# Optimization experiments

Measured on AMD Instinct MI355X. Metric: run time of the kernel, lower is better.

The kernel has to match this reference:

```python
import jax, jax.numpy as jnp
import numpy as np

N_NODES = 100000


def gcn_conv(x, W, b, src, dst, n):
    # PyG GCNConv: linear transform, add self-loops, symmetric degree norm, scatter-add, bias
    h = x @ W                                      # [n, d_out]
    loop = jnp.arange(n, dtype=src.dtype)
    s = jnp.concatenate([src, loop])               # [E + n]
    d = jnp.concatenate([dst, loop])
    deg = jax.ops.segment_sum(jnp.ones_like(d, dtype=h.dtype), d, num_segments=n)
    dinv = jnp.where(deg > 0, jax.lax.rsqrt(deg), 0.0)
    norm = dinv[s] * dinv[d]                       # [E + n]
    msg = h[s] * norm[:, None]                     # gather + scale
    out = jax.ops.segment_sum(msg, d, num_segments=n)  # scatter-add over targets
    return out + b


def setup_inputs() -> dict:
    key = jax.random.key(0)
    ks = jax.random.split(key, 8)
    n, c_in, hid, c_out = N_NODES, 256, 128, 64
    x = jax.random.normal(ks[0], (n, c_in), dtype=jnp.float32)
    edge_index = jax.random.randint(ks[1], (2, 1600000), 0, n, dtype=jnp.int64)
    s = 0.1
    return {
        "x": x,
        "edge_index": edge_index,
        "W1": jax.random.normal(ks[2], (c_in, hid), dtype=jnp.float32) * s,
        "b1": jnp.zeros((hid,), dtype=jnp.float32),
        "Wmu": jax.random.normal(ks[3], (hid, c_out), dtype=jnp.float32) * s,
        "bmu": jnp.zeros((c_out,), dtype=jnp.float32),
        "Wlv": jax.random.normal(ks[4], (hid, c_out), dtype=jnp.float32) * s,
        "blv": jnp.zeros((c_out,), dtype=jnp.float32),
    }


def reference(x, edge_index, W1, b1, Wmu, bmu, Wlv, blv):
    n = x.shape[0]
    src, dst = edge_index[0], edge_index[1]
    h = jax.nn.relu(gcn_conv(x, W1, b1, src, dst, n))
    mu = gcn_conv(h, Wmu, bmu, src, dst, n)
    logvar = gcn_conv(h, Wlv, blv, src, dst, n)
    return mu, logvar
```

## Files before the change

### kernel.cpp

```cpp
#include <hip/hip_runtime.h>


#define C_IN  256
#define HID   128
#define C_OUT 64
#define NBUCK 1024
#define P1WGS 256

typedef __attribute__((ext_vector_type(8))) short bf16x8;
typedef __attribute__((ext_vector_type(4))) float f32x4;

__device__ inline unsigned short f2bf(float f) {
  unsigned u = __float_as_uint(f);
  unsigned r = u + 0x7FFF + ((u >> 16) & 1);
  return (unsigned short)(r >> 16);
}
__device__ inline float bflo(unsigned v) { return __uint_as_float(v << 16); }
__device__ inline float bfhi(unsigned v) { return __uint_as_float(v & 0xFFFF0000u); }

__global__ __launch_bounds__(256) void k_bin_count(const int* __restrict__ dst,
                                                   int* __restrict__ histmat, int E) {
  __shared__ int h[NBUCK];
  int tid = threadIdx.x;
  for (int i = tid; i < NBUCK; i += 256) h[i] = 0;
  __syncthreads();
  for (int e = blockIdx.x * 256 + tid; e < E; e += P1WGS * 256)
    atomicAdd(&h[dst[e] >> 7], 1);
  __syncthreads();
  for (int i = tid; i < NBUCK; i += 256)
    histmat[blockIdx.x * NBUCK + i] = h[i];
}

__global__ __launch_bounds__(256) void k_col_scan(int* __restrict__ histmat,
                                                  int* __restrict__ bucket_tot) {
  __shared__ int sh[P1WGS];
  int b = blockIdx.x;
  int t = threadIdx.x;
  int v = histmat[t * NBUCK + b];
  sh[t] = v; __syncthreads();
  for (int ofs = 1; ofs < P1WGS; ofs <<= 1) {
    int add = (t >= ofs) ? sh[t - ofs] : 0;
    __syncthreads();
    sh[t] += add;
    __syncthreads();
  }
  histmat[t * NBUCK + b] = sh[t] - v;
  if (t == P1WGS - 1) bucket_tot[b] = sh[t];
}

__global__ void k_bucket_scan(const int* __restrict__ bucket_tot,
                              int* __restrict__ bucket_start, int E) {
  __shared__ int sh[NBUCK];
  int t = threadIdx.x;
  int v = bucket_tot[t];
  sh[t] = v; __syncthreads();
  for (int ofs = 1; ofs < NBUCK; ofs <<= 1) {
    int add = (t >= ofs) ? sh[t - ofs] : 0;
    __syncthreads();
    sh[t] += add;
    __syncthreads();
  }
  bucket_start[t] = sh[t] - v;
  if (t == NBUCK - 1) bucket_start[NBUCK] = E;
}

__global__ __launch_bounds__(256) void k_bin_scatter(const int* __restrict__ src,
                                                     const int* __restrict__ dst,
                                                     const int* __restrict__ histmat,
                                                     const int* __restrict__ bucket_start,
                                                     unsigned* __restrict__ binned, int E) {
  __shared__ int cur[NBUCK];
  int tid = threadIdx.x;
  for (int i = tid; i < NBUCK; i += 256)
    cur[i] = bucket_start[i] + histmat[blockIdx.x * NBUCK + i];
  __syncthreads();
  for (int e = blockIdx.x * 256 + tid; e < E; e += P1WGS * 256) {
    int d = dst[e];
    int pos = atomicAdd(&cur[d >> 7], 1);
    binned[pos] = (unsigned)src[e] | ((unsigned)(d & 127) << 17);
  }
}

__global__ __launch_bounds__(256) void k_bucket_csr(const unsigned* __restrict__ binned,
                                                    const int* __restrict__ bucket_start,
                                                    int* __restrict__ row_start,
                                                    float* __restrict__ dinv,
                                                    int* __restrict__ csr_src,
                                                    int n, int E) {
  __shared__ int h[128], ls[128], c[128];
  int b = blockIdx.x, t = threadIdx.x;
  int start = bucket_start[b], end = bucket_start[b + 1];
  if (t < 128) h[t] = 0;
  __syncthreads();
  for (int e = start + t; e < end; e += 256)
    atomicAdd(&h[binned[e] >> 17], 1);
  __syncthreads();
  if (t < 128) ls[t] = h[t];
  __syncthreads();
  for (int ofs = 1; ofs < 128; ofs <<= 1) {
    int add = (t < 128 && t >= ofs) ? ls[t - ofs] : 0;
    __syncthreads();
    if (t < 128) ls[t] += add;
    __syncthreads();
  }
  if (t < 128) {
    int excl = ls[t] - h[t];
    ls[t] = excl;
    c[t] = excl;
    int node = b * 128 + t;
    if (node < n) {
      row_start[node] = start + excl;
      dinv[node] = rsqrtf((float)h[t] + 1.0f);
    }
  }
  if (b == 0 && t == 0) row_start[n] = E;
  __syncthreads();
  for (int e = start + t; e < end; e += 256) {
    unsigned v = binned[e];
    int pos = start + atomicAdd(&c[v >> 17], 1);
    csr_src[pos] = (int)(v & 0x1FFFF);
  }
}

__global__ void k_prep(const float* __restrict__ W1, const float* __restrict__ Wmu,
                       const float* __restrict__ Wlv,
                       unsigned short* __restrict__ bswz1,
                       unsigned short* __restrict__ bswz2,
                       unsigned* __restrict__ p1z, unsigned* __restrict__ p2z) {
  int idx = blockIdx.x * 256 + threadIdx.x;
  if (idx < 4096) {
    int L = idx & 63, t = (idx >> 6) & 7, s = idx >> 9;
    const float* srcp = W1 + (size_t)(s * 32 + ((L >> 4) << 3)) * 128 + t * 16 + (L & 15);
    unsigned short* dstp = bswz1 + (size_t)idx * 8;
#pragma unroll
    for (int j = 0; j < 8; j++) dstp[j] = f2bf(srcp[(size_t)j * 128]);
  } else if (idx < 6144) {
    int id2 = idx - 4096;
    int L = id2 & 63, t = (id2 >> 6) & 7, s = id2 >> 9;
    int nn = t * 16 + (L & 15);
    int k0 = s * 32 + ((L >> 4) << 3);
    const float* W = (nn < C_OUT) ? (Wmu + nn) : (Wlv + (nn - C_OUT));
    unsigned short* dstp = bswz2 + (size_t)id2 * 8;
#pragma unroll
    for (int j = 0; j < 8; j++) dstp[j] = f2bf(W[(size_t)(k0 + j) * C_OUT]);
  } else if (idx < 6208) {
    p1z[idx - 6144] = 0u;
  } else if (idx < 6272) {
    p2z[idx - 6208] = 0u;
  }
}

template <typename AT, int K>
__global__ __launch_bounds__(256) void k_gemm_mfma(const AT* __restrict__ A,
                                                   const unsigned short* __restrict__ bswz,
                                                   unsigned short* __restrict__ C,
                                                   const float* __restrict__ dinv,
                                                   int M) {
  constexpr int NS = K / 32;
  int wave = threadIdx.x >> 6, lane = threadIdx.x & 63;
  int m0 = blockIdx.x * 64 + wave * 16;
  int lrow = lane & 15, lq = lane >> 4;
  int arow = m0 + lrow;
  bool rv = arow < M;
  const AT* ap = A + (size_t)(rv ? arow : 0) * K + lq * 8;

  auto loadA = [&](int s) -> bf16x8 {
    if (sizeof(AT) == 4) {
      const float* af = (const float*)ap + s * 32;
      float4 u0 = rv ? *(const float4*)(af) : float4{0, 0, 0, 0};
      float4 u1 = rv ? *(const float4*)(af + 4) : float4{0, 0, 0, 0};
      union { unsigned short us[8]; bf16x8 v; } tmp;
      tmp.us[0] = f2bf(u0.x); tmp.us[1] = f2bf(u0.y);
      tmp.us[2] = f2bf(u0.z); tmp.us[3] = f2bf(u0.w);
      tmp.us[4] = f2bf(u1.x); tmp.us[5] = f2bf(u1.y);
      tmp.us[6] = f2bf(u1.z); tmp.us[7] = f2bf(u1.w);
      return tmp.v;
    } else {
      const unsigned short* ab = (const unsigned short*)ap + s * 32;
      return rv ? *(const bf16x8*)(ab) : (bf16x8)(short)0;
    }
  };

  f32x4 acc[8];
#pragma unroll
  for (int t = 0; t < 8; t++) acc[t] = (f32x4){0.f, 0.f, 0.f, 0.f};

  bf16x8 a_cur = loadA(0);
  bf16x8 b_cur[8];
#pragma unroll
  for (int t = 0; t < 8; t++)
    b_cur[t] = *(const bf16x8*)(bswz + lane * 8 + t * 512);

#pragma unroll
  for (int s = 0; s < NS; ++s) {
    bf16x8 a_nxt = a_cur;
    bf16x8 b_nxt[8];
    if (s + 1 < NS) {
      a_nxt = loadA(s + 1);
      const unsigned short* bp = bswz + (size_t)(s + 1) * 4096 + lane * 8;
#pragma unroll
      for (int t = 0; t < 8; t++) b_nxt[t] = *(const bf16x8*)(bp + t * 512);
    }
#pragma unroll
    for (int t = 0; t < 8; t++)
      acc[t] = __builtin_amdgcn_mfma_f32_16x16x32_bf16(a_cur, b_cur[t], acc[t], 0, 0, 0);
    a_cur = a_nxt;
    if (s + 1 < NS) {
#pragma unroll
      for (int t = 0; t < 8; t++) b_cur[t] = b_nxt[t];
    }
  }
#pragma unroll
  for (int i = 0; i < 4; i++) {
    int rr = m0 + lq * 4 + i;
    if (rr < M) {
      float dsc = dinv[rr];
      unsigned short* cp = C + (size_t)rr * 128 + lrow;
#pragma unroll
      for (int t = 0; t < 8; t++) cp[t * 16] = f2bf(acc[t][i] * dsc);
    }
  }
}

#define AGG_V4_BODY                                                                 \
  int tid = threadIdx.x;                                                            \
  int wid4 = blockIdx.x * 4 + (tid >> 6);                           \
  int lane = tid & 63;                                                              \
  int li = lane & 15;                                                               \
  int node = (wid4 << 2) + (lane >> 4);                                             \
  int rs = 0, re = -1;                                                              \
  if (node < n) { rs = row_start[node]; re = row_start[node + 1]; }                 \
  int mc = re - rs + 1;                                       \
  mc = max(mc, __shfl_xor(mc, 16, 64));                                             \
  mc = max(mc, __shfl_xor(mc, 32, 64));                                             \
  int maxcnt = __builtin_amdgcn_readfirstlane(mc);                                  \
  const char* pb = (const char*)p;                                                  \
  unsigned loff = (unsigned)(li << 4);                                              \
  int vb = (lane & 48) << 2;          \
  float acc0 = 0.f, acc1 = 0.f, acc2 = 0.f, acc3 = 0.f;                             \
  float acc4 = 0.f, acc5 = 0.f, acc6 = 0.f, acc7 = 0.f;                             \
  for (int t0 = 0; t0 < maxcnt; t0 += 16) {                                         \
    int s = rs + t0 + li;                                                           \
    int sl = n;                                                       \
    if (s < re) sl = csr[s];                                                        \
    else if (s == re) sl = node;                                     \
    unsigned o[16];                                                                 \
    _Pragma("unroll")                                                               \
    for (int k = 0; k < 16; ++k)                                                    \
      o[k] = ((unsigned)__builtin_amdgcn_ds_bpermute(vb + (k << 2), sl)) << 8;      \
    uint4 v[16];                                                                    \
    _Pragma("unroll")                                                               \
    for (int k = 0; k < 16; ++k)                                                    \
      v[k] = *(const uint4*)(pb + (o[k] + loff));                                   \
    _Pragma("unroll")                                                               \
    for (int k = 0; k < 16; ++k) {                                                  \
      acc0 += bflo(v[k].x); acc1 += bfhi(v[k].x);                                   \
      acc2 += bflo(v[k].y); acc3 += bfhi(v[k].y);                                   \
      acc4 += bflo(v[k].z); acc5 += bfhi(v[k].z);                                   \
      acc6 += bflo(v[k].w); acc7 += bfhi(v[k].w);                                   \
    }                                                                               \
  }

__global__ __launch_bounds__(256) void k_agg_relu_bf(
    const unsigned short* __restrict__ p, const float* __restrict__ dinv,
    const int* __restrict__ row_start, const int* __restrict__ csr,
    const float* __restrict__ bias, unsigned short* __restrict__ h, int n) {
  AGG_V4_BODY
  if (node < n) {
    float di = dinv[node];
    float4 ba = *(const float4*)(bias + (li << 3));
    float4 bb = *(const float4*)(bias + (li << 3) + 4);
    float r0 = fmaxf(acc0 * di + ba.x, 0.f);
    float r1 = fmaxf(acc1 * di + ba.y, 0.f);
    float r2 = fmaxf(acc2 * di + ba.z, 0.f);
    float r3 = fmaxf(acc3 * di + ba.w, 0.f);
    float r4 = fmaxf(acc4 * di + bb.x, 0.f);
    float r5 = fmaxf(acc5 * di + bb.y, 0.f);
    float r6 = fmaxf(acc6 * di + bb.z, 0.f);
    float r7 = fmaxf(acc7 * di + bb.w, 0.f);
    uint4 u;
    u.x = (unsigned)f2bf(r0) | ((unsigned)f2bf(r1) << 16);
    u.y = (unsigned)f2bf(r2) | ((unsigned)f2bf(r3) << 16);
    u.z = (unsigned)f2bf(r4) | ((unsigned)f2bf(r5) << 16);
    u.w = (unsigned)f2bf(r6) | ((unsigned)f2bf(r7) << 16);
    *(uint4*)((char*)h + (((size_t)node) << 8) + loff) = u;
  }
}

__global__ __launch_bounds__(256) void k_agg_out_bf(
    const unsigned short* __restrict__ p, const float* __restrict__ dinv,
    const int* __restrict__ row_start, const int* __restrict__ csr,
    const float* __restrict__ bmu, const float* __restrict__ blv,
    float* __restrict__ out, int n) {
  AGG_V4_BODY
  if (node < n) {
    float di = dinv[node];
    const float* bp = (li < 8) ? (bmu + (li << 3)) : (blv + ((li - 8) << 3));
    float* op = (li < 8) ? (out + (size_t)node * C_OUT + (li << 3))
                         : (out + (size_t)(n + node) * C_OUT + ((li - 8) << 3));
    float4 b0 = *(const float4*)(bp);
    float4 b1 = *(const float4*)(bp + 4);
    float4 o0 = {acc0 * di + b0.x, acc1 * di + b0.y,
                 acc2 * di + b0.z, acc3 * di + b0.w};
    float4 o1 = {acc4 * di + b1.x, acc5 * di + b1.y,
                 acc6 * di + b1.z, acc7 * di + b1.w};
    *(float4*)op = o0;
    *(float4*)(op + 4) = o1;
  }
}

extern "C" void kernel_launch(void* const* d_in, const int* in_sizes, int n_in,
                              void* d_out, int out_size, void* d_ws, size_t ws_size,
                              hipStream_t stream) {
  const float* x   = (const float*)d_in[0];
  const int*   ei  = (const int*)d_in[1];
  const float* W1  = (const float*)d_in[2];
  const float* b1  = (const float*)d_in[3];
  const float* Wmu = (const float*)d_in[4];
  const float* bmu = (const float*)d_in[5];
  const float* Wlv = (const float*)d_in[6];
  const float* blv = (const float*)d_in[7];
  float* out = (float*)d_out;

  const int n = in_sizes[0] / C_IN;
  const int E = in_sizes[1] / 2;
  const int* src = ei;
  const int* dst = ei + E;

  char* w = (char*)d_ws;
  auto alloc = [&](size_t bytes) -> void* {
    void* pp = (void*)w;
    w += (bytes + 255) & ~(size_t)255;
    return pp;
  };
  float*          dinv       = (float*)alloc((size_t)n * 4);
  int*            row_start  = (int*)alloc((size_t)(n + 1) * 4);
  int*            histmat    = (int*)alloc((size_t)P1WGS * NBUCK * 4);
  int*            bucket_tot = (int*)alloc((size_t)NBUCK * 4);
  int*            bucket_st  = (int*)alloc((size_t)(NBUCK + 1) * 4);
  unsigned*       binned     = (unsigned*)alloc((size_t)E * 4);
  int*            csr_src    = (int*)alloc((size_t)E * 4);
  unsigned short* bswz1      = (unsigned short*)alloc((size_t)C_IN * 128 * 2);
  unsigned short* bswz2      = (unsigned short*)alloc((size_t)HID * 128 * 2);
  unsigned short* p1         = (unsigned short*)alloc((size_t)(n + 1) * 128 * 2);
  unsigned short* hbuf       = (unsigned short*)alloc((size_t)n * 128 * 2);
  unsigned short* p2         = (unsigned short*)alloc((size_t)(n + 1) * 128 * 2);
  (void)ws_size; (void)n_in; (void)out_size;

  const int TB = 256;
  const int gemm_bks = (n + 63) / 64;
  const int agg_bks = (n + 15) / 16;
  const int nbk_csr = (n + 127) / 128;

  k_bin_count<<<P1WGS, TB, 0, stream>>>(dst, histmat, E);
  k_col_scan<<<NBUCK, TB, 0, stream>>>(histmat, bucket_tot);
  k_bucket_scan<<<1, NBUCK, 0, stream>>>(bucket_tot, bucket_st, E);
  k_bin_scatter<<<P1WGS, TB, 0, stream>>>(src, dst, histmat, bucket_st, binned, E);
  k_bucket_csr<<<nbk_csr, TB, 0, stream>>>(binned, bucket_st, row_start, dinv,
                                           csr_src, n, E);

  k_prep<<<25, 256, 0, stream>>>(W1, Wmu, Wlv, bswz1, bswz2,
                                 (unsigned*)(p1 + (size_t)n * 128),
                                 (unsigned*)(p2 + (size_t)n * 128));

  k_gemm_mfma<float, C_IN><<<gemm_bks, TB, 0, stream>>>(x, bswz1, p1, dinv, n);
  k_agg_relu_bf<<<agg_bks, TB, 0, stream>>>(p1, dinv, row_start, csr_src, b1, hbuf, n);

  k_gemm_mfma<unsigned short, HID><<<gemm_bks, TB, 0, stream>>>(hbuf, bswz2, p2, dinv, n);
  k_agg_out_bf<<<agg_bks, TB, 0, stream>>>(p2, dinv, row_start, csr_src, bmu, blv, out, n);
}
```

Before: 402.9 us.

## Fuse layer-1 aggregation with second GEMM and merge prep into bin count

```diff
diff --git a/kernel.cpp b/kernel.cpp
--- a/kernel.cpp
+++ b/kernel.cpp
@@ -18,17 +18,45 @@
 __device__ inline float bflo(unsigned v) { return __uint_as_float(v << 16); }
 __device__ inline float bfhi(unsigned v) { return __uint_as_float(v & 0xFFFF0000u); }
 
-__global__ __launch_bounds__(256) void k_bin_count(const int* __restrict__ dst,
-                                                   int* __restrict__ histmat, int E) {
+__global__ __launch_bounds__(256) void k_count_prep(
+    const int* __restrict__ dst, int* __restrict__ histmat, int E,
+    const float* __restrict__ W1, const float* __restrict__ Wmu,
+    const float* __restrict__ Wlv,
+    unsigned short* __restrict__ bswz1, unsigned short* __restrict__ bswz2,
+    unsigned* __restrict__ p1z, unsigned* __restrict__ p2z) {
   __shared__ int h[NBUCK];
   int tid = threadIdx.x;
-  for (int i = tid; i < NBUCK; i += 256) h[i] = 0;
-  __syncthreads();
-  for (int e = blockIdx.x * 256 + tid; e < E; e += P1WGS * 256)
-    atomicAdd(&h[dst[e] >> 7], 1);
-  __syncthreads();
-  for (int i = tid; i < NBUCK; i += 256)
-    histmat[blockIdx.x * NBUCK + i] = h[i];
+  if (blockIdx.x < P1WGS) {
+    for (int i = tid; i < NBUCK; i += 256) h[i] = 0;
+    __syncthreads();
+    for (int e = blockIdx.x * 256 + tid; e < E; e += P1WGS * 256)
+      atomicAdd(&h[dst[e] >> 7], 1);
+    __syncthreads();
+    for (int i = tid; i < NBUCK; i += 256)
+      histmat[blockIdx.x * NBUCK + i] = h[i];
+    return;
+  }
+  int idx = (blockIdx.x - P1WGS) * 256 + tid;
+  if (idx < 4096) {
+    int L = idx & 63, t = (idx >> 6) & 7, s = idx >> 9;
+    const float* srcp = W1 + (size_t)(s * 32 + ((L >> 4) << 3)) * 128 + t * 16 + (L & 15);
+    unsigned short* dstp = bswz1 + (size_t)idx * 8;
+#pragma unroll
+    for (int j = 0; j < 8; j++) dstp[j] = f2bf(srcp[(size_t)j * 128]);
+  } else if (idx < 6144) {
+    int id2 = idx - 4096;
+    int L = id2 & 63, t = (id2 >> 6) & 7, s = id2 >> 9;
+    int nn = t * 16 + (L & 15);
+    int k0 = s * 32 + ((L >> 4) << 3);
+    const float* W = (nn < C_OUT) ? (Wmu + nn) : (Wlv + (nn - C_OUT));
+    unsigned short* dstp = bswz2 + (size_t)id2 * 8;
+#pragma unroll
+    for (int j = 0; j < 8; j++) dstp[j] = f2bf(W[(size_t)(k0 + j) * C_OUT]);
+  } else if (idx < 6208) {
+    p1z[idx - 6144] = 0u;
+  } else if (idx < 6272) {
+    p2z[idx - 6208] = 0u;
+  }
 }
 
 __global__ __launch_bounds__(256) void k_col_scan(int* __restrict__ histmat,
@@ -119,34 +147,6 @@
     unsigned v = binned[e];
     int pos = start + atomicAdd(&c[v >> 17], 1);
     csr_src[pos] = (int)(v & 0x1FFFF);
-  }
-}
-
-__global__ void k_prep(const float* __restrict__ W1, const float* __restrict__ Wmu,
-                       const float* __restrict__ Wlv,
-                       unsigned short* __restrict__ bswz1,
-                       unsigned short* __restrict__ bswz2,
-                       unsigned* __restrict__ p1z, unsigned* __restrict__ p2z) {
-  int idx = blockIdx.x * 256 + threadIdx.x;
-  if (idx < 4096) {
-    int L = idx & 63, t = (idx >> 6) & 7, s = idx >> 9;
-    const float* srcp = W1 + (size_t)(s * 32 + ((L >> 4) << 3)) * 128 + t * 16 + (L & 15);
-    unsigned short* dstp = bswz1 + (size_t)idx * 8;
-#pragma unroll
-    for (int j = 0; j < 8; j++) dstp[j] = f2bf(srcp[(size_t)j * 128]);
-  } else if (idx < 6144) {
-    int id2 = idx - 4096;
-    int L = id2 & 63, t = (id2 >> 6) & 7, s = id2 >> 9;
-    int nn = t * 16 + (L & 15);
-    int k0 = s * 32 + ((L >> 4) << 3);
-    const float* W = (nn < C_OUT) ? (Wmu + nn) : (Wlv + (nn - C_OUT));
-    unsigned short* dstp = bswz2 + (size_t)id2 * 8;
-#pragma unroll
-    for (int j = 0; j < 8; j++) dstp[j] = f2bf(W[(size_t)(k0 + j) * C_OUT]);
-  } else if (idx < 6208) {
-    p1z[idx - 6144] = 0u;
-  } else if (idx < 6272) {
-    p2z[idx - 6208] = 0u;
   }
 }
 
@@ -261,29 +261,59 @@
     }                                                                               \
   }
 
-__global__ __launch_bounds__(256) void k_agg_relu_bf(
+__global__ __launch_bounds__(256) void k_agg_gemm2(
     const unsigned short* __restrict__ p, const float* __restrict__ dinv,
     const int* __restrict__ row_start, const int* __restrict__ csr,
-    const float* __restrict__ bias, unsigned short* __restrict__ h, int n) {
+    const float* __restrict__ bias, const unsigned short* __restrict__ bswz2,
+    unsigned short* __restrict__ p2, int n) {
+  __shared__ unsigned short hs[16][136];
   AGG_V4_BODY
-  if (node < n) {
-    float di = dinv[node];
-    float4 ba = *(const float4*)(bias + (li << 3));
-    float4 bb = *(const float4*)(bias + (li << 3) + 4);
-    float r0 = fmaxf(acc0 * di + ba.x, 0.f);
-    float r1 = fmaxf(acc1 * di + ba.y, 0.f);
-    float r2 = fmaxf(acc2 * di + ba.z, 0.f);
-    float r3 = fmaxf(acc3 * di + ba.w, 0.f);
-    float r4 = fmaxf(acc4 * di + bb.x, 0.f);
-    float r5 = fmaxf(acc5 * di + bb.y, 0.f);
-    float r6 = fmaxf(acc6 * di + bb.z, 0.f);
-    float r7 = fmaxf(acc7 * di + bb.w, 0.f);
-    uint4 u;
-    u.x = (unsigned)f2bf(r0) | ((unsigned)f2bf(r1) << 16);
-    u.y = (unsigned)f2bf(r2) | ((unsigned)f2bf(r3) << 16);
-    u.z = (unsigned)f2bf(r4) | ((unsigned)f2bf(r5) << 16);
-    u.w = (unsigned)f2bf(r6) | ((unsigned)f2bf(r7) << 16);
-    *(uint4*)((char*)h + (((size_t)node) << 8) + loff) = u;
+  int rwg = ((tid >> 6) << 2) + (lane >> 4);
+  {
+    uint4 u = {0u, 0u, 0u, 0u};
+    if (node < n) {
+      float di = dinv[node];
+      float4 ba = *(const float4*)(bias + (li << 3));
+      float4 bb = *(const float4*)(bias + (li << 3) + 4);
+      float r0 = fmaxf(acc0 * di + ba.x, 0.f);
+      float r1 = fmaxf(acc1 * di + ba.y, 0.f);
+      float r2 = fmaxf(acc2 * di + ba.z, 0.f);
+      float r3 = fmaxf(acc3 * di + ba.w, 0.f);
+      float r4 = fmaxf(acc4 * di + bb.x, 0.f);
+      float r5 = fmaxf(acc5 * di + bb.y, 0.f);
+      float r6 = fmaxf(acc6 * di + bb.z, 0.f);
+      float r7 = fmaxf(acc7 * di + bb.w, 0.f);
+      u.x = (unsigned)f2bf(r0) | ((unsigned)f2bf(r1) << 16);
+      u.y = (unsigned)f2bf(r2) | ((unsigned)f2bf(r3) << 16);
+      u.z = (unsigned)f2bf(r4) | ((unsigned)f2bf(r5) << 16);
+      u.w = (unsigned)f2bf(r6) | ((unsigned)f2bf(r7) << 16);
+    }
+    *(uint4*)(&hs[rwg][li << 3]) = u;
+  }
+  __syncthreads();
+
+  int w = tid >> 6;
+  int lrow = lane & 15, lq = lane >> 4;
+  f32x4 g0 = (f32x4){0.f, 0.f, 0.f, 0.f};
+  f32x4 g1 = (f32x4){0.f, 0.f, 0.f, 0.f};
+#pragma unroll
+  for (int s = 0; s < 4; ++s) {
+    bf16x8 af = *(const bf16x8*)(&hs[lrow][(lq << 3) + s * 32]);
+    const unsigned short* bp = bswz2 + s * 4096 + (w * 2) * 512 + lane * 8;
+    bf16x8 bf0 = *(const bf16x8*)(bp);
+    bf16x8 bf1 = *(const bf16x8*)(bp + 512);
+    g0 = __builtin_amdgcn_mfma_f32_16x16x32_bf16(af, bf0, g0, 0, 0, 0);
+    g1 = __builtin_amdgcn_mfma_f32_16x16x32_bf16(af, bf1, g1, 0, 0, 0);
+  }
+#pragma unroll
+  for (int i = 0; i < 4; ++i) {
+    int rr = blockIdx.x * 16 + (lq << 2) + i;
+    if (rr < n) {
+      float dsc = dinv[rr];
+      unsigned short* cp = p2 + (size_t)rr * 128 + lrow;
+      cp[(w * 2) * 16]     = f2bf(g0[i] * dsc);
+      cp[(w * 2 + 1) * 16] = f2bf(g1[i] * dsc);
+    }
   }
 }
 
@@ -343,7 +373,6 @@
   unsigned short* bswz1      = (unsigned short*)alloc((size_t)C_IN * 128 * 2);
   unsigned short* bswz2      = (unsigned short*)alloc((size_t)HID * 128 * 2);
   unsigned short* p1         = (unsigned short*)alloc((size_t)(n + 1) * 128 * 2);
-  unsigned short* hbuf       = (unsigned short*)alloc((size_t)n * 128 * 2);
   unsigned short* p2         = (unsigned short*)alloc((size_t)(n + 1) * 128 * 2);
   (void)ws_size; (void)n_in; (void)out_size;
 
@@ -352,20 +381,20 @@
   const int agg_bks = (n + 15) / 16;
   const int nbk_csr = (n + 127) / 128;
 
-  k_bin_count<<<P1WGS, TB, 0, stream>>>(dst, histmat, E);
+  k_count_prep<<<P1WGS + 25, TB, 0, stream>>>(dst, histmat, E, W1, Wmu, Wlv,
+                                              bswz1, bswz2,
+                                              (unsigned*)(p1 + (size_t)n * 128),
+                                              (unsigned*)(p2 + (size_t)n * 128));
   k_col_scan<<<NBUCK, TB, 0, stream>>>(histmat, bucket_tot);
   k_bucket_scan<<<1, NBUCK, 0, stream>>>(bucket_tot, bucket_st, E);
   k_bin_scatter<<<P1WGS, TB, 0, stream>>>(src, dst, histmat, bucket_st, binned, E);
   k_bucket_csr<<<nbk_csr, TB, 0, stream>>>(binned, bucket_st, row_start, dinv,
                                            csr_src, n, E);
 
-  k_prep<<<25, 256, 0, stream>>>(W1, Wmu, Wlv, bswz1, bswz2,
-                                 (unsigned*)(p1 + (size_t)n * 128),
-                                 (unsigned*)(p2 + (size_t)n * 128));
-
   k_gemm_mfma<float, C_IN><<<gemm_bks, TB, 0, stream>>>(x, bswz1, p1, dinv, n);
-  k_agg_relu_bf<<<agg_bks, TB, 0, stream>>>(p1, dinv, row_start, csr_src, b1, hbuf, n);
-
-  k_gemm_mfma<unsigned short, HID><<<gemm_bks, TB, 0, stream>>>(hbuf, bswz2, p2, dinv, n);
+
+  k_agg_gemm2<<<agg_bks, TB, 0, stream>>>(p1, dinv, row_start, csr_src, b1,
+                                          bswz2, p2, n);
+
   k_agg_out_bf<<<agg_bks, TB, 0, stream>>>(p2, dinv, row_start, csr_src, bmu, blv, out, n);
 }
```

Measured after the change: 395.5 us. About the same (-1.8%).
